# Performance work log

Measured on AMD Instinct MI355X. Metric: run time of the kernel, lower is better.

## Reference

```python
import jax, jax.numpy as jnp
import numpy as np

QK_DIM = 1024
V_DIM = 1024
NUM_HEADS = 16
B, L = 4, 2048


def setup_inputs() -> dict:
    key = jax.random.key(0)
    ks = jax.random.split(key, 12)
    s_in = 1.0 / np.sqrt(QK_DIM)
    inp = {
        "q": jax.random.normal(ks[0], (B, L, QK_DIM), jnp.float32),
        "k": jax.random.normal(ks[1], (B, L, QK_DIM), jnp.float32),
        "v": jax.random.normal(ks[2], (B, L, V_DIM), jnp.float32),
        "Wq": jax.random.uniform(ks[3], (QK_DIM, QK_DIM), jnp.float32, -s_in, s_in),
        "bq": jnp.zeros((QK_DIM,), jnp.float32),
        "Wk": jax.random.uniform(ks[4], (QK_DIM, QK_DIM), jnp.float32, -s_in, s_in),
        "bk": jnp.zeros((QK_DIM,), jnp.float32),
        "Wv": jax.random.uniform(ks[5], (V_DIM, V_DIM), jnp.float32, -s_in, s_in),
        "bv": jnp.zeros((V_DIM,), jnp.float32),
        "Wo": jax.random.uniform(ks[6], (V_DIM, V_DIM), jnp.float32, -s_in, s_in),
        "bo": jnp.zeros((V_DIM,), jnp.float32),
        "offset": jnp.float32(0.0),
    }
    return inp


def _split_heads(x, n_heads):
    b, l, d = x.shape
    return x.reshape(b, l, n_heads, d // n_heads).transpose(0, 2, 1, 3)  # [B,H,L,Dh]


def reference(q, k, v, Wq, bq, Wk, bk, Wv, bv, Wo, bo, offset):
    # in-projections (nn.Linear: x @ W.T + b; here W stored as [in,out])
    q = q @ Wq + bq
    k = k @ Wk + bk
    v = v @ Wv + bv
    scale = (QK_DIM // NUM_HEADS) ** (-0.5)
    q = q * scale
    qh = _split_heads(q, NUM_HEADS)  # [B,H,L,Dh]
    kh = _split_heads(k, NUM_HEADS)
    vh = _split_heads(v, NUM_HEADS)
    scores = jnp.einsum("bhqd,bhkd->bhqk", qh, kh) + offset
    A = jax.nn.softmax(scores, axis=-1)  # attn_dropout is identity in eval
    out = jnp.einsum("bhqk,bhkd->bhqd", A, vh)
    out = out.transpose(0, 2, 1, 3).reshape(B, L, V_DIM)  # merge heads
    out = out @ Wo + bo  # out projection; seq_dropout identity in eval
    return out
```

## Files before the change

kernel.cpp:

```cpp
#include <hip/hip_runtime.h>
#include <hip/hip_bf16.h>
#include <stdint.h>

typedef __bf16 bf16;
typedef __bf16 bf16x8 __attribute__((ext_vector_type(8)));
typedef __bf16 bf16x4v __attribute__((ext_vector_type(4)));
typedef float f32x4 __attribute__((ext_vector_type(4)));
typedef uint32_t u32;
typedef u32 u32x2 __attribute__((ext_vector_type(2)));
typedef u32 u32x4 __attribute__((ext_vector_type(4)));

__device__ __forceinline__ void gld_lds16(const void* g, void* l) {
  __builtin_amdgcn_global_load_lds(
      (const __attribute__((address_space(1))) void*)g,
      (__attribute__((address_space(3))) void*)l, 16, 0, 0);
}

__device__ __forceinline__ f32x4 mfma16(bf16x8 a, bf16x8 b, f32x4 c) {
  return __builtin_amdgcn_mfma_f32_16x16x32_bf16(a, b, c, 0, 0, 0);
}

__device__ __forceinline__ u32 cvtpk_bf16(float lo, float hi) {
  u32 r;
  asm("v_cvt_pk_bf16_f32 %0, %1, %2" : "=v"(r) : "v"(lo), "v"(hi));
  return r;
}

__device__ __forceinline__ float fexp2(float x) {
#if __has_builtin(__builtin_amdgcn_exp2f)
  return __builtin_amdgcn_exp2f(x);
#else
  return exp2f(x);
#endif
}

__global__ void wt_cvt4_k(const float* __restrict__ W0, const float* __restrict__ W1,
                          const float* __restrict__ W2, const float* __restrict__ W3,
                          bf16* __restrict__ T0, bf16* __restrict__ T1,
                          bf16* __restrict__ T2, bf16* __restrict__ T3) {
  const float* W = (blockIdx.z == 0) ? W0 : (blockIdx.z == 1) ? W1
                  : (blockIdx.z == 2) ? W2 : W3;
  bf16* WT = (blockIdx.z == 0) ? T0 : (blockIdx.z == 1) ? T1
            : (blockIdx.z == 2) ? T2 : T3;
  __shared__ float t[32][33];
  int tx = threadIdx.x, ty = threadIdx.y;
  int bx = blockIdx.x * 32, by = blockIdx.y * 32;
#pragma unroll
  for (int j = 0; j < 32; j += 8)
    t[ty + j][tx] = W[(size_t)(by + ty + j) * 1024 + bx + tx];
  __syncthreads();
#pragma unroll
  for (int j = 0; j < 32; j += 8)
    WT[(size_t)(bx + ty + j) * 1024 + by + tx] = (bf16)t[tx][ty + j];
}

__global__ __launch_bounds__(256, 2) void gemmf_k(
    const float* __restrict__ Aq, const float* __restrict__ Ak, const float* __restrict__ Av,
    const bf16* __restrict__ WTq, const bf16* __restrict__ WTk, const bf16* __restrict__ WTv,
    const float* __restrict__ bq, const float* __restrict__ bk, const float* __restrict__ bv,
    bf16* __restrict__ Qa, bf16* __restrict__ Ka, bf16* __restrict__ VTa, float qscale) {
  constexpr int K = 1024, BM = 128, BK = 64;
  constexpr int NT = K / BK;
  __shared__ char lds[2][2][BM * BK * 2];
  const int lane = threadIdx.x & 63, w = threadIdx.x >> 6;
  const int y = blockIdx.y;
  const float* A   = (y == 0) ? Aq : (y == 1) ? Ak : Av;
  const bf16* WT   = (y == 0) ? WTq : (y == 1) ? WTk : WTv;
  const float* bias = (y == 0) ? bq : (y == 1) ? bk : bv;
  const float scale = (y == 0) ? qscale : 1.0f;
  const int nwg = gridDim.x;
  int bid = (int)blockIdx.x;
  bid = (bid & 7) * (nwg >> 3) + (bid >> 3);
  const int bn = bid & 7;
  const int bm = bid >> 3;
  const int wm = (w & 1) * 64, wn = (w >> 1) * 64;
  const int l7 = lane & 7, sl = lane >> 3;
  const int sw = l7 ^ sl;

  const char* gA = (const char*)(A + (size_t)bm * BM * K);
  const char* gB = (const char*)(WT + (size_t)bn * BM * K);

  auto stageB = [&](int buf, int kt) {
    char* lB = lds[buf][1];
#pragma unroll
    for (int i = 0; i < 4; ++i) {
      int row = w * 32 + i * 8 + sl;
      gld_lds16(gB + (size_t)row * 2048 + (size_t)kt * 128 + (size_t)l7 * 16,
                lB + (w * 32 + i * 8) * 128);
    }
  };
  auto stage_loadA = [&](int kt, f32x4 (&a0)[4], f32x4 (&a1)[4]) {
#pragma unroll
    for (int i = 0; i < 4; ++i) {
      int row = w * 32 + i * 8 + sl;
      const char* src = gA + (size_t)row * 4096 + (size_t)kt * 256 + (size_t)l7 * 32;
      a0[i] = *(const f32x4*)src;
      a1[i] = *(const f32x4*)(src + 16);
    }
  };
  auto stage_writeA = [&](int buf, f32x4 (&a0)[4], f32x4 (&a1)[4]) {
    char* lA = lds[buf][0];
#pragma unroll
    for (int i = 0; i < 4; ++i) {
      int row = w * 32 + i * 8 + sl;
      u32x4 pk;
      pk[0] = cvtpk_bf16(a0[i][0], a0[i][1]);
      pk[1] = cvtpk_bf16(a0[i][2], a0[i][3]);
      pk[2] = cvtpk_bf16(a1[i][0], a1[i][1]);
      pk[3] = cvtpk_bf16(a1[i][2], a1[i][3]);
      *(bf16x8*)(lA + row * 128 + sw * 16) = __builtin_bit_cast(bf16x8, pk);
    }
  };

  f32x4 a0[4], a1[4];
  stageB(0, 0);
  stage_loadA(0, a0, a1);
  stage_writeA(0, a0, a1);

  f32x4 acc[4][4] = {};
  for (int kt = 0; kt < NT; ++kt) {
    __syncthreads();
    if (kt + 1 < NT) {
      stageB((kt + 1) & 1, kt + 1);
      stage_loadA(kt + 1, a0, a1);
    }
    const char* lA = lds[kt & 1][0];
    const char* lB = lds[kt & 1][1];
    bf16x8 af[4][2], bfr[4][2];
#pragma unroll
    for (int mi = 0; mi < 4; ++mi)
#pragma unroll
      for (int c = 0; c < 2; ++c) {
        int row = wm + mi * 16 + (lane & 15);
        int ch = (c * 4 + (lane >> 4)) ^ (lane & 7);
        af[mi][c] = *(const bf16x8*)(lA + row * 128 + ch * 16);
      }
#pragma unroll
    for (int ni = 0; ni < 4; ++ni)
#pragma unroll
      for (int c = 0; c < 2; ++c) {
        int row = wn + ni * 16 + (lane & 15);
        int ch = c * 4 + (lane >> 4);
        bfr[ni][c] = *(const bf16x8*)(lB + row * 128 + ch * 16);
      }
#pragma unroll
    for (int mi = 0; mi < 4; ++mi)
#pragma unroll
      for (int ni = 0; ni < 4; ++ni) {
        acc[mi][ni] = mfma16(af[mi][0], bfr[ni][0], acc[mi][ni]);
        acc[mi][ni] = mfma16(af[mi][1], bfr[ni][1], acc[mi][ni]);
      }
    if (kt + 1 < NT) stage_writeA((kt + 1) & 1, a0, a1);
  }

#pragma unroll
  for (int ni = 0; ni < 4; ++ni) {
    int col = bn * 128 + wn + ni * 16 + (lane & 15);
    float bv2 = bias[col];
    int h = col >> 6, dh = col & 63;
    if (y != 2) {
      bf16* out = (y == 0) ? Qa : Ka;
#pragma unroll
      for (int mi = 0; mi < 4; ++mi)
#pragma unroll
        for (int r = 0; r < 4; ++r) {
          int row = bm * BM + wm + mi * 16 + (lane >> 4) * 4 + r;
          int b = row >> 11, li = row & 2047;
          out[(((size_t)(b * 16 + h) * 2048 + li) << 6) + dh] =
              (bf16)((acc[mi][ni][r] + bv2) * scale);
        }
    } else {
      bf16* out = VTa;
#pragma unroll
      for (int mi = 0; mi < 4; ++mi)
#pragma unroll
        for (int r = 0; r < 4; ++r) {
          int row = bm * BM + wm + mi * 16 + (lane >> 4) * 4 + r;
          int b = row >> 11, li = row & 2047;
          out[(((size_t)(b * 16 + h) * 64 + dh) << 11) + li] =
              (bf16)(acc[mi][ni][r] + bv2);
        }
    }
  }
}

__global__ __launch_bounds__(256, 2) void gemm_out_k(
    const bf16* __restrict__ A, const bf16* __restrict__ WT,
    const float* __restrict__ bias, float* __restrict__ Cout) {
  constexpr int K = 1024, N = 1024, BM = 128, BK = 64;
  constexpr int NT = K / BK;
  __shared__ char lds[2][2][BM * BK * 2];
  const int lane = threadIdx.x & 63, w = threadIdx.x >> 6;
  const int nwg = gridDim.x;
  int bid = (int)blockIdx.x;
  bid = (bid & 7) * (nwg >> 3) + (bid >> 3);
  const int bn = bid & 7;
  const int bm = bid >> 3;
  const int wm = (w & 1) * 64, wn = (w >> 1) * 64;

  const char* gA = (const char*)(A + (size_t)bm * BM * K);
  const char* gB = (const char*)(WT + (size_t)bn * BM * K);

  auto stage = [&](int buf, int kt) {
    char* lA = lds[buf][0];
    char* lB = lds[buf][1];
#pragma unroll
    for (int i = 0; i < 4; ++i) {
      int row = w * 32 + i * 8 + (lane >> 3);
      size_t rb = (size_t)row * (K * 2) + (size_t)kt * (BK * 2) + (size_t)(lane & 7) * 16;
      gld_lds16(gA + rb, lA + (w * 32 + i * 8) * 128);
      gld_lds16(gB + rb, lB + (w * 32 + i * 8) * 128);
    }
  };

  f32x4 acc[4][4] = {};
  stage(0, 0);
  for (int kt = 0; kt < NT; ++kt) {
    __syncthreads();
    if (kt + 1 < NT) stage((kt + 1) & 1, kt + 1);
    const char* lA = lds[kt & 1][0];
    const char* lB = lds[kt & 1][1];
    bf16x8 af[4][2], bfr[4][2];
#pragma unroll
    for (int mi = 0; mi < 4; ++mi)
#pragma unroll
      for (int c = 0; c < 2; ++c) {
        int row = wm + mi * 16 + (lane & 15);
        int ch = c * 4 + (lane >> 4);
        af[mi][c] = *(const bf16x8*)(lA + row * 128 + ch * 16);
      }
#pragma unroll
    for (int ni = 0; ni < 4; ++ni)
#pragma unroll
      for (int c = 0; c < 2; ++c) {
        int row = wn + ni * 16 + (lane & 15);
        int ch = c * 4 + (lane >> 4);
        bfr[ni][c] = *(const bf16x8*)(lB + row * 128 + ch * 16);
      }
#pragma unroll
    for (int mi = 0; mi < 4; ++mi)
#pragma unroll
      for (int ni = 0; ni < 4; ++ni) {
        acc[mi][ni] = mfma16(af[mi][0], bfr[ni][0], acc[mi][ni]);
        acc[mi][ni] = mfma16(af[mi][1], bfr[ni][1], acc[mi][ni]);
      }
  }

#pragma unroll
  for (int ni = 0; ni < 4; ++ni) {
    int col = bn * 128 + wn + ni * 16 + (lane & 15);
    float bv = bias[col];
#pragma unroll
    for (int mi = 0; mi < 4; ++mi)
#pragma unroll
      for (int r = 0; r < 4; ++r) {
        int row = bm * BM + wm + mi * 16 + (lane >> 4) * 4 + r;
        Cout[(size_t)row * N + col] = acc[mi][ni][r] + bv;
      }
  }
}

__global__ __launch_bounds__(256, 3) void attn_mfma_k(
    const bf16* __restrict__ Q, const bf16* __restrict__ Kg,
    const bf16* __restrict__ VT, bf16* __restrict__ AO) {
  constexpr int L = 2048, DH = 64, NT = L / 64;
  __shared__ char ldsK[2][8192];
  __shared__ char ldsVT[2][8192];
  __shared__ char ldsP[4][2][2048];
  const int lane = threadIdx.x & 63, w = threadIdx.x >> 6;
  const int nwg = gridDim.x;
  int bid = (int)blockIdx.x;
  bid = (bid & 7) * (nwg >> 3) + (bid >> 3);
  const int bh = bid >> 4;
  const int q0 = (bid & 15) * 128;
  const int b = bh >> 4, h = bh & 15;
  const int l7 = lane & 7;
  const int q15 = lane & 15, g4 = lane >> 4;
  const int sl = lane >> 3;
  const int sw = l7 ^ sl;

  const bf16* Qbase = Q + ((size_t)bh * L + q0 + w * 32) * DH;
  bf16x8 qf[2][2];
#pragma unroll
  for (int rt = 0; rt < 2; ++rt)
#pragma unroll
    for (int c = 0; c < 2; ++c)
      qf[rt][c] = *(const bf16x8*)(Qbase + (size_t)(rt * 16 + q15) * DH +
                                   (c * 4 + g4) * 8);

  const char* Kp  = (const char*)(Kg + (size_t)bh * L * DH);
  const char* VTp = (const char*)(VT + (size_t)bh * DH * L);

  auto stage = [&](int buf, int kt) {
#pragma unroll
    for (int c = 0; c < 2; ++c) {
      int chunk = w * 2 + c;
      int row = chunk * 8 + sl;
      gld_lds16(Kp + (size_t)kt * 8192 + (size_t)row * 128 + sw * 16,
                ldsK[buf] + chunk * 1024);
      gld_lds16(VTp + (size_t)row * 4096 + (size_t)kt * 128 + sw * 16,
                ldsVT[buf] + chunk * 1024);
    }
  };

  f32x4 o[2][4] = {};
  float lpart[2] = {0.f, 0.f};

  stage(0, 0);
  for (int kt = 0; kt < NT; ++kt) {
    __syncthreads();
    if (kt + 1 < NT) stage((kt + 1) & 1, kt + 1);
    const char* lK  = ldsK[kt & 1];
    const char* lVT = ldsVT[kt & 1];

    bf16x8 kf[4][2];
#pragma unroll
    for (int sub = 0; sub < 4; ++sub)
#pragma unroll
      for (int c = 0; c < 2; ++c) {
        int key = sub * 16 + q15;
        int ch = (c * 4 + g4) ^ l7;
        kf[sub][c] = *(const bf16x8*)(lK + key * 128 + ch * 16);
      }

#pragma unroll
    for (int rt = 0; rt < 2; ++rt) {
      f32x4 s[4];
#pragma unroll
      for (int sub = 0; sub < 4; ++sub) {
        f32x4 acc = {};
        acc = mfma16(kf[sub][0], qf[rt][0], acc);
        acc = mfma16(kf[sub][1], qf[rt][1], acc);
        s[sub] = acc;
      }
#pragma unroll
      for (int sub = 0; sub < 4; ++sub) {
        float p0 = fexp2(s[sub][0]), p1 = fexp2(s[sub][1]);
        float p2 = fexp2(s[sub][2]), p3 = fexp2(s[sub][3]);
        lpart[rt] += (p0 + p1) + (p2 + p3);
        u32x2 pw;
        pw[0] = cvtpk_bf16(p0, p1);
        pw[1] = cvtpk_bf16(p2, p3);
        bf16x4v pv = __builtin_bit_cast(bf16x4v, pw);
        int chs = (2 * sub + (g4 >> 1)) ^ l7;
        *(bf16x4v*)(ldsP[w][rt] + q15 * 128 + chs * 16 + (g4 & 1) * 8) = pv;
      }
    }

    asm volatile("s_waitcnt lgkmcnt(0)" ::: "memory");
    __builtin_amdgcn_sched_barrier(0);

    bf16x8 pf[2][2];
#pragma unroll
    for (int rt = 0; rt < 2; ++rt)
#pragma unroll
      for (int c = 0; c < 2; ++c) {
        int ch = (c * 4 + g4) ^ l7;
        pf[rt][c] = *(const bf16x8*)(ldsP[w][rt] + q15 * 128 + ch * 16);
      }

#pragma unroll
    for (int n = 0; n < 4; ++n) {
      int dim = n * 16 + q15;
      bf16x8 vf[2];
#pragma unroll
      for (int c = 0; c < 2; ++c) {
        int ch = (c * 4 + g4) ^ l7;
        vf[c] = *(const bf16x8*)(lVT + dim * 128 + ch * 16);
      }
#pragma unroll
      for (int rt = 0; rt < 2; ++rt) {
        o[rt][n] = mfma16(pf[rt][0], vf[0], o[rt][n]);
        o[rt][n] = mfma16(pf[rt][1], vf[1], o[rt][n]);
      }
    }
  }

  float lf[2];
#pragma unroll
  for (int rt = 0; rt < 2; ++rt) {
    float v = lpart[rt];
    v += __shfl_xor(v, 16, 64);
    v += __shfl_xor(v, 32, 64);
    lf[rt] = v;
  }

#pragma unroll
  for (int rt = 0; rt < 2; ++rt) {
    float inv[4];
#pragma unroll
    for (int r = 0; r < 4; ++r)
      inv[r] = 1.f / __shfl(lf[rt], g4 * 4 + r, 64);
#pragma unroll
    for (int n = 0; n < 4; ++n) {
      int col = h * 64 + n * 16 + q15;
#pragma unroll
      for (int r = 0; r < 4; ++r) {
        int qrow = q0 + w * 32 + rt * 16 + g4 * 4 + r;
        AO[((size_t)b * L + qrow) * 1024 + col] = (bf16)(o[rt][n][r] * inv[r]);
      }
    }
  }
}

extern "C" void kernel_launch(void* const* d_in, const int* in_sizes, int n_in,
                              void* d_out, int out_size, void* d_ws, size_t ws_size,
                              hipStream_t stream) {
  (void)in_sizes; (void)n_in; (void)out_size;
  const size_t MB = 1u << 20;
  if (ws_size < 73 * MB) return;

  const float* q  = (const float*)d_in[0];
  const float* k  = (const float*)d_in[1];
  const float* v  = (const float*)d_in[2];
  const float* Wq = (const float*)d_in[3];
  const float* bq = (const float*)d_in[4];
  const float* Wk = (const float*)d_in[5];
  const float* bk = (const float*)d_in[6];
  const float* Wv = (const float*)d_in[7];
  const float* bv = (const float*)d_in[8];
  const float* Wo = (const float*)d_in[9];
  const float* bo = (const float*)d_in[10];

  char* ws = (char*)d_ws;
  bf16* Qa  = (bf16*)(ws + 0 * MB);
  bf16* Ka  = (bf16*)(ws + 16 * MB);
  bf16* VTa = (bf16*)(ws + 32 * MB);
  bf16* AO  = (bf16*)(ws + 48 * MB);
  bf16* WqT = (bf16*)(ws + 64 * MB);
  bf16* WkT = (bf16*)(ws + 66 * MB);
  bf16* WvT = (bf16*)(ws + 68 * MB);
  bf16* WoT = (bf16*)(ws + 70 * MB);

  dim3 tb(32, 8);
  wt_cvt4_k<<<dim3(32, 32, 4), tb, 0, stream>>>(Wq, Wk, Wv, Wo, WqT, WkT, WvT, WoT);

  gemmf_k<<<dim3(512, 3), 256, 0, stream>>>(
      q, k, v, WqT, WkT, WvT, bq, bk, bv, Qa, Ka, VTa,
      0.125f * 1.4426950408889634f);

  attn_mfma_k<<<1024, 256, 0, stream>>>(Qa, Ka, VTa, AO);

  gemm_out_k<<<512, 256, 0, stream>>>(AO, WoT, bo, (float*)d_out);
}
```

Before: 202.3 us.

## Load QKV-projection weight fragments directly from global memory, halve LDS use

The fused QKV projection GEMM no longer stages the transposed weight tile through LDS. Each wave now reads its B fragments straight from global memory (served by L2) every k-step. This halves the LDS footprint, and the launch bound is raised to 4 blocks per CU to allow more occupancy. The cost is more global/L2 traffic, since every wave re-reads its weight slice, plus load latency that is exposed right before the MFMAs with no prefetch.

```diff
diff --git a/kernel.cpp b/kernel.cpp
--- a/kernel.cpp
+++ b/kernel.cpp
@@ -54,14 +54,14 @@
     WT[(size_t)(bx + ty + j) * 1024 + by + tx] = (bf16)t[tx][ty + j];
 }
 
-__global__ __launch_bounds__(256, 2) void gemmf_k(
+__global__ __launch_bounds__(256, 4) void gemmf_k(
     const float* __restrict__ Aq, const float* __restrict__ Ak, const float* __restrict__ Av,
     const bf16* __restrict__ WTq, const bf16* __restrict__ WTk, const bf16* __restrict__ WTv,
     const float* __restrict__ bq, const float* __restrict__ bk, const float* __restrict__ bv,
     bf16* __restrict__ Qa, bf16* __restrict__ Ka, bf16* __restrict__ VTa, float qscale) {
   constexpr int K = 1024, BM = 128, BK = 64;
   constexpr int NT = K / BK;
-  __shared__ char lds[2][2][BM * BK * 2];
+  __shared__ char lds[2][BM * BK * 2];
   const int lane = threadIdx.x & 63, w = threadIdx.x >> 6;
   const int y = blockIdx.y;
   const float* A   = (y == 0) ? Aq : (y == 1) ? Ak : Av;
@@ -74,21 +74,13 @@
   const int bn = bid & 7;
   const int bm = bid >> 3;
   const int wm = (w & 1) * 64, wn = (w >> 1) * 64;
+  const int q15 = lane & 15, g4 = lane >> 4;
   const int l7 = lane & 7, sl = lane >> 3;
   const int sw = l7 ^ sl;
 
   const char* gA = (const char*)(A + (size_t)bm * BM * K);
-  const char* gB = (const char*)(WT + (size_t)bn * BM * K);
-
-  auto stageB = [&](int buf, int kt) {
-    char* lB = lds[buf][1];
-#pragma unroll
-    for (int i = 0; i < 4; ++i) {
-      int row = w * 32 + i * 8 + sl;
-      gld_lds16(gB + (size_t)row * 2048 + (size_t)kt * 128 + (size_t)l7 * 16,
-                lB + (w * 32 + i * 8) * 128);
-    }
-  };
+  const bf16* gBw = WT + (size_t)(bn * 128 + wn + q15) * K;
+
   auto stage_loadA = [&](int kt, f32x4 (&a0)[4], f32x4 (&a1)[4]) {
 #pragma unroll
     for (int i = 0; i < 4; ++i) {
@@ -99,7 +91,7 @@
     }
   };
   auto stage_writeA = [&](int buf, f32x4 (&a0)[4], f32x4 (&a1)[4]) {
-    char* lA = lds[buf][0];
+    char* lA = lds[buf];
 #pragma unroll
     for (int i = 0; i < 4; ++i) {
       int row = w * 32 + i * 8 + sl;
@@ -113,35 +105,28 @@
   };
 
   f32x4 a0[4], a1[4];
-  stageB(0, 0);
   stage_loadA(0, a0, a1);
   stage_writeA(0, a0, a1);
 
   f32x4 acc[4][4] = {};
   for (int kt = 0; kt < NT; ++kt) {
     __syncthreads();
-    if (kt + 1 < NT) {
-      stageB((kt + 1) & 1, kt + 1);
-      stage_loadA(kt + 1, a0, a1);
-    }
-    const char* lA = lds[kt & 1][0];
-    const char* lB = lds[kt & 1][1];
-    bf16x8 af[4][2], bfr[4][2];
+    if (kt + 1 < NT) stage_loadA(kt + 1, a0, a1);
+    bf16x8 bfr[4][2];
+#pragma unroll
+    for (int ni = 0; ni < 4; ++ni)
+#pragma unroll
+      for (int c = 0; c < 2; ++c)
+        bfr[ni][c] = *(const bf16x8*)(gBw + (size_t)ni * 16 * K + kt * 64 + (c * 4 + g4) * 8);
+    const char* lA = lds[kt & 1];
+    bf16x8 af[4][2];
 #pragma unroll
     for (int mi = 0; mi < 4; ++mi)
 #pragma unroll
       for (int c = 0; c < 2; ++c) {
-        int row = wm + mi * 16 + (lane & 15);
-        int ch = (c * 4 + (lane >> 4)) ^ (lane & 7);
+        int row = wm + mi * 16 + q15;
+        int ch = (c * 4 + g4) ^ (lane & 7);
         af[mi][c] = *(const bf16x8*)(lA + row * 128 + ch * 16);
-      }
-#pragma unroll
-    for (int ni = 0; ni < 4; ++ni)
-#pragma unroll
-      for (int c = 0; c < 2; ++c) {
-        int row = wn + ni * 16 + (lane & 15);
-        int ch = c * 4 + (lane >> 4);
-        bfr[ni][c] = *(const bf16x8*)(lB + row * 128 + ch * 16);
       }
 #pragma unroll
     for (int mi = 0; mi < 4; ++mi)
@@ -155,7 +140,7 @@
 
 #pragma unroll
   for (int ni = 0; ni < 4; ++ni) {
-    int col = bn * 128 + wn + ni * 16 + (lane & 15);
+    int col = bn * 128 + wn + ni * 16 + q15;
     float bv2 = bias[col];
     int h = col >> 6, dh = col & 63;
     if (y != 2) {
@@ -164,7 +149,7 @@
       for (int mi = 0; mi < 4; ++mi)
 #pragma unroll
         for (int r = 0; r < 4; ++r) {
-          int row = bm * BM + wm + mi * 16 + (lane >> 4) * 4 + r;
+          int row = bm * BM + wm + mi * 16 + g4 * 4 + r;
           int b = row >> 11, li = row & 2047;
           out[(((size_t)(b * 16 + h) * 2048 + li) << 6) + dh] =
               (bf16)((acc[mi][ni][r] + bv2) * scale);
@@ -175,7 +160,7 @@
       for (int mi = 0; mi < 4; ++mi)
 #pragma unroll
         for (int r = 0; r < 4; ++r) {
-          int row = bm * BM + wm + mi * 16 + (lane >> 4) * 4 + r;
+          int row = bm * BM + wm + mi * 16 + g4 * 4 + r;
           int b = row >> 11, li = row & 2047;
           out[(((size_t)(b * 16 + h) * 64 + dh) << 11) + li] =
               (bf16)(acc[mi][ni][r] + bv2);
```

Measured after the change: 260.9 us. 29.0% more time.
